# Kernel tuning notes

Measured on AMD Instinct MI355X. Metric: run time of the kernel, lower is better.

Reference implementation:

```python
import jax, jax.numpy as jnp
import numpy as np

D_MODEL = 768
NUM_HEADS = 12
HEAD_DIM = D_MODEL // NUM_HEADS
SEQ = 4096
BATCH = 1


def setup_inputs() -> dict:
    key = jax.random.key(0)
    ks = jax.random.split(key, 6)
    scale = 1.0 / np.sqrt(D_MODEL)
    x = jax.random.normal(ks[0], (BATCH, SEQ, D_MODEL), dtype=jnp.float32)
    mask = jnp.tril(jnp.ones((SEQ, SEQ), dtype=bool))[None, None]  # [1,1,S,S] causal
    Wq = jax.random.normal(ks[1], (D_MODEL, D_MODEL), dtype=jnp.float32) * scale
    Wk = jax.random.normal(ks[2], (D_MODEL, D_MODEL), dtype=jnp.float32) * scale
    Wv = jax.random.normal(ks[3], (D_MODEL, D_MODEL), dtype=jnp.float32) * scale
    Wo = jax.random.normal(ks[4], (D_MODEL, D_MODEL), dtype=jnp.float32) * scale
    bo = jax.random.normal(ks[5], (D_MODEL,), dtype=jnp.float32) * 0.01
    return {"x": x, "mask": mask, "Wq": Wq, "Wk": Wk, "Wv": Wv, "Wo": Wo, "bo": bo}


def _rope_tables(seq_len, head_dim, dtype):
    # inv_freq over even dims; emb = cat(freqs, freqs) but only the first half
    # participates in the well-defined rotation (x1/x2 have head_dim//2 channels)
    inv_freq = 1.0 / (10000.0 ** (jnp.arange(0, head_dim, 2, dtype=dtype) / head_dim))
    t = jnp.arange(seq_len, dtype=dtype)
    freqs = t[:, None] * inv_freq[None, :]  # [S, head_dim//2]
    return jnp.cos(freqs), jnp.sin(freqs)


def _apply_rotary(xh, cos, sin):
    # xh: [B,H,S,hd]; cos/sin: [S, hd//2]
    x1 = xh[..., ::2]
    x2 = xh[..., 1::2]
    # faithful to source: concatenated (not interleaved) rotated halves
    return jnp.concatenate([x1 * cos - x2 * sin, x1 * sin + x2 * cos], axis=-1)


def reference(x, mask, Wq, Wk, Wv, Wo, bo):
    B, S, D = x.shape
    H, hd = NUM_HEADS, HEAD_DIM
    def split_heads(y):
        return y.reshape(B, S, H, hd).transpose(0, 2, 1, 3)  # [B,H,S,hd]
    q = split_heads(x @ Wq.T)
    k = split_heads(x @ Wk.T)
    v = split_heads(x @ Wv.T)
    cos, sin = _rope_tables(S, hd, x.dtype)
    q = _apply_rotary(q, cos, sin)
    k = _apply_rotary(k, cos, sin)
    scores = jnp.einsum('bhqd,bhkd->bhqk', q, k) / jnp.sqrt(jnp.asarray(hd, x.dtype))
    scores = jnp.where(mask, scores, jnp.asarray(-1e9, x.dtype))
    attn = jax.nn.softmax(scores, axis=-1)  # dropout is identity in eval
    out = jnp.einsum('bhqk,bhkd->bhqd', attn, v)
    out = out.transpose(0, 2, 1, 3).reshape(B, S, D)
    return out @ Wo.T + bo
```

## Files before the change

kernel.cpp:

```cpp
#include <hip/hip_runtime.h>
#include <hip/hip_bf16.h>
#include <math.h>

#define SEQ 4096
#define DM  768
#define NH  12
#define HD  64
#define PER ((size_t)NH * SEQ * HD)
#define XN  ((size_t)SEQ * DM)
#define WN  ((size_t)DM * DM)

typedef __attribute__((ext_vector_type(8))) short bf16x8;
typedef __attribute__((ext_vector_type(4))) short s16x4;
typedef __attribute__((ext_vector_type(4))) float f32x4;

#define MFMA(a, b, c) __builtin_amdgcn_mfma_f32_16x16x32_bf16((a), (b), (c), 0, 0, 0)

#if __has_builtin(__builtin_amdgcn_exp2f)
#define EXP2(x) __builtin_amdgcn_exp2f(x)
#else
#define EXP2(x) exp2f(x)
#endif

#define SWZ(row, blk) (((row) << 6) + ((((blk) ^ ((row) & 7))) << 3))

__device__ __forceinline__ unsigned short f2b(float f) {
    unsigned int u = __float_as_uint(f);
    u += 0x7FFFu + ((u >> 16) & 1u);
    return (unsigned short)(u >> 16);
}

__global__ __launch_bounds__(256) void prep_kernel(
    const float* __restrict__ x,  const float* __restrict__ wq,
    const float* __restrict__ wk, const float* __restrict__ wv,
    const float* __restrict__ wo,
    unsigned short* __restrict__ dstbase, float2* __restrict__ rope)
{
    const float* srcs[5] = {x, wq, wk, wv, wo};
    const size_t n4s[5]  = {XN / 4, WN / 4, WN / 4, WN / 4, WN / 4};
    unsigned short* d = dstbase;
    for (int rg = 0; rg < 5; ++rg) {
        const float4* s4 = (const float4*)srcs[rg];
        s16x4* d4 = (s16x4*)d;
        for (size_t i = (size_t)blockIdx.x * 256 + threadIdx.x; i < n4s[rg];
             i += (size_t)gridDim.x * 256) {
            const float4 v = s4[i];
            s16x4 p;
            p.x = (short)f2b(v.x); p.y = (short)f2b(v.y);
            p.z = (short)f2b(v.z); p.w = (short)f2b(v.w);
            d4[i] = p;
        }
        d += n4s[rg] * 4;
    }
    for (int g = blockIdx.x * 256 + threadIdx.x; g < 131072; g += gridDim.x * 256) {
        const int row = g >> 5, fi = g & 31;
        const float invf = expf(-(float)fi * 0.28782313662425576f);
        float sn, cs;
        sincosf((float)row * invf, &sn, &cs);
        rope[row * 32 + fi] = make_float2(cs, sn);
    }
}

__global__ __launch_bounds__(256) void qkv_mfma(
    const float* __restrict__ x,  const unsigned short* __restrict__ xb,
    const float* __restrict__ Wq, const float* __restrict__ Wk, const float* __restrict__ Wv,
    const unsigned short* __restrict__ Wqb, const unsigned short* __restrict__ Wkb,
    const unsigned short* __restrict__ Wvb,
    const float2* __restrict__ rope,
    unsigned short* __restrict__ Qo, unsigned short* __restrict__ Ko,
    unsigned short* __restrict__ Vo, int fast)
{
    __shared__ __align__(16) unsigned short Xs[2][4096];
    __shared__ __align__(16) unsigned short Ws[2][4096];
    __shared__ unsigned short VL[64 * 66];

    const int t    = threadIdx.x;
    const int w    = t >> 6;
    const int lane = t & 63;
    const int quad = lane >> 4;
    const int l16  = lane & 15;

    const int nt_b = blockIdx.y;
    const float* W; const unsigned short* Wb; int region;
    if (nt_b < 12)      { W = Wq; Wb = Wqb; region = 0; }
    else if (nt_b < 24) { W = Wk; Wb = Wkb; region = 1; }
    else                { W = Wv; Wb = Wvb; region = 2; }
    const int h  = nt_b % 12;
    const int s0 = blockIdx.x * 64;
    const int n0 = h * 64;

    f32x4 acc[4] = {{0,0,0,0},{0,0,0,0},{0,0,0,0},{0,0,0,0}};
    const int prow = t >> 3, pblk = t & 7;

    bf16x8 xr0, xr1, wr0, wr1;
    if (fast) {
        xr0 = *(const bf16x8*)&xb[(size_t)(s0 + prow) * DM + pblk * 8];
        xr1 = *(const bf16x8*)&xb[(size_t)(s0 + prow + 32) * DM + pblk * 8];
        wr0 = *(const bf16x8*)&Wb[(size_t)(n0 + prow) * DM + pblk * 8];
        wr1 = *(const bf16x8*)&Wb[(size_t)(n0 + prow + 32) * DM + pblk * 8];
        *(bf16x8*)&Xs[0][SWZ(prow, pblk)]      = xr0;
        *(bf16x8*)&Xs[0][SWZ(prow + 32, pblk)] = xr1;
        *(bf16x8*)&Ws[0][SWZ(prow, pblk)]      = wr0;
        *(bf16x8*)&Ws[0][SWZ(prow + 32, pblk)] = wr1;
    } else {
        for (int e = t; e < 1024; e += 256) {
            const int row = e >> 4, c4 = e & 15;
            const int off = SWZ(row, c4 >> 1) + (c4 & 1) * 4;
            const float4 xv = *(const float4*)&x[(size_t)(s0 + row) * DM + c4 * 4];
            s16x4 px; px.x = (short)f2b(xv.x); px.y = (short)f2b(xv.y);
            px.z = (short)f2b(xv.z); px.w = (short)f2b(xv.w);
            *(s16x4*)&Xs[0][off] = px;
            const float4 wv = *(const float4*)&W[(size_t)(n0 + row) * DM + c4 * 4];
            s16x4 pw; pw.x = (short)f2b(wv.x); pw.y = (short)f2b(wv.y);
            pw.z = (short)f2b(wv.z); pw.w = (short)f2b(wv.w);
            *(s16x4*)&Ws[0][off] = pw;
        }
    }
    __syncthreads();

    for (int kt = 0; kt < 12; ++kt) {
        const unsigned short* Xb  = Xs[kt & 1];
        const unsigned short* Wbt = Ws[kt & 1];
        if (fast && kt < 11) {
            const int k0 = (kt + 1) * 64;
            xr0 = *(const bf16x8*)&xb[(size_t)(s0 + prow) * DM + k0 + pblk * 8];
            xr1 = *(const bf16x8*)&xb[(size_t)(s0 + prow + 32) * DM + k0 + pblk * 8];
            wr0 = *(const bf16x8*)&Wb[(size_t)(n0 + prow) * DM + k0 + pblk * 8];
            wr1 = *(const bf16x8*)&Wb[(size_t)(n0 + prow + 32) * DM + k0 + pblk * 8];
        }
        const bf16x8 a0 = *(const bf16x8*)&Xb[SWZ(16 * w + l16, quad)];
        const bf16x8 a1 = *(const bf16x8*)&Xb[SWZ(16 * w + l16, 4 + quad)];
        #pragma unroll
        for (int nt = 0; nt < 4; ++nt) {
            const bf16x8 b0 = *(const bf16x8*)&Wbt[SWZ(16 * nt + l16, quad)];
            const bf16x8 b1 = *(const bf16x8*)&Wbt[SWZ(16 * nt + l16, 4 + quad)];
            acc[nt] = MFMA(a0, b0, acc[nt]);
            acc[nt] = MFMA(a1, b1, acc[nt]);
        }
        if (kt < 11) {
            const int nb = (kt + 1) & 1;
            if (fast) {
                *(bf16x8*)&Xs[nb][SWZ(prow, pblk)]      = xr0;
                *(bf16x8*)&Xs[nb][SWZ(prow + 32, pblk)] = xr1;
                *(bf16x8*)&Ws[nb][SWZ(prow, pblk)]      = wr0;
                *(bf16x8*)&Ws[nb][SWZ(prow + 32, pblk)] = wr1;
            } else {
                const int k0 = (kt + 1) * 64;
                for (int e = t; e < 1024; e += 256) {
                    const int row = e >> 4, c4 = e & 15;
                    const int off = SWZ(row, c4 >> 1) + (c4 & 1) * 4;
                    const float4 xv = *(const float4*)&x[(size_t)(s0 + row) * DM + k0 + c4 * 4];
                    s16x4 px; px.x = (short)f2b(xv.x); px.y = (short)f2b(xv.y);
                    px.z = (short)f2b(xv.z); px.w = (short)f2b(xv.w);
                    *(s16x4*)&Xs[nb][off] = px;
                    const float4 wv = *(const float4*)&W[(size_t)(n0 + row) * DM + k0 + c4 * 4];
                    s16x4 pw; pw.x = (short)f2b(wv.x); pw.y = (short)f2b(wv.y);
                    pw.z = (short)f2b(wv.z); pw.w = (short)f2b(wv.w);
                    *(s16x4*)&Ws[nb][off] = pw;
                }
            }
        }
        __syncthreads();
    }

    const size_t headoff = (size_t)h * SEQ * HD;
    if (region <= 1) {
        unsigned short* dst = (region == 0) ? Qo : Ko;
        const float qsc = (region == 0) ? 0.18033688011112042f : 1.0f;
        #pragma unroll
        for (int nt = 0; nt < 4; ++nt)
            #pragma unroll
            for (int r = 0; r < 4; ++r) {
                const int srow = s0 + 16 * w + quad * 4 + r;
                const int d  = nt * 16 + l16;
                const int fi = d >> 1;
                const float own = acc[nt][r] * qsc;
                const float oth = __shfl_xor(own, 1);
                float cs, sn;
                if (fast) {
                    const float2 t2 = rope[srow * 32 + fi];
                    cs = t2.x; sn = t2.y;
                } else {
                    const float invf = expf(-(float)fi * 0.28782313662425576f);
                    sincosf((float)srow * invf, &sn, &cs);
                }
                const float val = (d & 1) ? (oth * sn + own * cs)
                                          : (own * cs - oth * sn);
                dst[headoff + (size_t)srow * HD + ((d & 1) ? 32 : 0) + fi] = f2b(val);
            }
    } else {
        #pragma unroll
        for (int nt = 0; nt < 4; ++nt)
            #pragma unroll
            for (int r = 0; r < 4; ++r)
                VL[(nt * 16 + l16) * 66 + 16 * w + quad * 4 + r] = f2b(acc[nt][r]);
        __syncthreads();
        for (int e = t; e < 2048; e += 256) {
            const int d = e >> 5, sp = e & 31;
            const unsigned int v = (unsigned int)VL[d * 66 + 2 * sp] |
                                   ((unsigned int)VL[d * 66 + 2 * sp + 1] << 16);
            *(unsigned int*)&Vo[headoff + (size_t)d * SEQ + s0 + 2 * sp] = v;
        }
    }
}

__global__ __launch_bounds__(256, 2) void attn_mfma(
    const unsigned short* __restrict__ Q,
    const unsigned short* __restrict__ K,
    const unsigned short* __restrict__ V,
    unsigned short* __restrict__ O)
{
    __shared__ __align__(16) unsigned char SM[53248];
    unsigned short* Kst = (unsigned short*)SM;
    unsigned short* Vt  = (unsigned short*)(SM + 16384);
    unsigned short* Ps  = (unsigned short*)(SM + 32768);
    float* ACC  = (float*)SM;
    float* ACC2 = (float*)(SM + 32768);
    float* Lx   = (float*)(SM + 51200);

    const int h    = blockIdx.y;
    const int q0   = (63 - blockIdx.x) * 64;
    const int t    = threadIdx.x;
    const int w    = t >> 6;
    const int lane = t & 63;
    const int quad = lane >> 4;
    const int l16  = lane & 15;
    const size_t headoff = (size_t)h * SEQ * HD;

    for (int e = t; e < 512; e += 256) {
        const int row = e >> 3, bp = e & 7, blk = bp ^ (row & 7);
        *(bf16x8*)&Kst[row * 64 + bp * 8] =
            *(const bf16x8*)&Q[headoff + (size_t)(q0 + row) * HD + blk * 8];
    }
    __syncthreads();
    bf16x8 aQ[4][2];
    #pragma unroll
    for (int qt = 0; qt < 4; ++qt)
        #pragma unroll
        for (int hh = 0; hh < 2; ++hh)
            aQ[qt][hh] = *(const bf16x8*)&Kst[SWZ(16 * qt + l16, 4 * hh + quad)];
    __syncthreads();

    bf16x8 kreg[4], vreg[4];
    #pragma unroll
    for (int i = 0; i < 4; ++i) {
        const int e = t + i * 256, row = e >> 3, bp = e & 7, blk = bp ^ (row & 7);
        kreg[i] = *(const bf16x8*)&K[headoff + (size_t)row * HD + blk * 8];
    }
    #pragma unroll
    for (int i = 0; i < 4; ++i) {
        const int e = t + i * 256, row = e >> 4, bp = e & 15, blk = bp ^ (row & 15);
        vreg[i] = *(const bf16x8*)&V[headoff + (size_t)row * SEQ + blk * 8];
    }
    #pragma unroll
    for (int i = 0; i < 4; ++i) {
        const int e = t + i * 256, row = e >> 3, bp = e & 7;
        *(bf16x8*)&Kst[row * 64 + bp * 8] = kreg[i];
    }
    #pragma unroll
    for (int i = 0; i < 4; ++i) {
        const int e = t + i * 256, row = e >> 4, bp = e & 15;
        *(bf16x8*)&Vt[row * 128 + bp * 8] = vreg[i];
    }
    __syncthreads();

    bf16x8 ones;
    #pragma unroll
    for (int i = 0; i < 8; ++i) ones[i] = (short)0x3F80;

    f32x4 oT[4][4];
    #pragma unroll
    for (int dt = 0; dt < 4; ++dt)
        #pragma unroll
        for (int qt = 0; qt < 4; ++qt) oT[dt][qt] = (f32x4){0,0,0,0};
    f32x4 lT[4] = {{0,0,0,0},{0,0,0,0},{0,0,0,0},{0,0,0,0}};

    unsigned short* usp = Ps + w * 2560;
    const int cmax = (q0 + 63) >> 7;

    for (int c = 0; c <= cmax; ++c) {
        const int k0 = c * 128;

        f32x4 sC[4][2];
        #pragma unroll
        for (int qt = 0; qt < 4; ++qt)
            #pragma unroll
            for (int kt = 0; kt < 2; ++kt) sC[qt][kt] = (f32x4){0,0,0,0};
        #pragma unroll
        for (int kt = 0; kt < 2; ++kt) {
            const int krow = 32 * w + 16 * kt + l16;
            #pragma unroll
            for (int hh = 0; hh < 2; ++hh) {
                const bf16x8 bK = *(const bf16x8*)&Kst[SWZ(krow, 4 * hh + quad)];
                #pragma unroll
                for (int qt = 0; qt < 4; ++qt)
                    sC[qt][kt] = MFMA(aQ[qt][hh], bK, sC[qt][kt]);
            }
        }

        if (c < cmax) {
            const int kn = k0 + 128;
            #pragma unroll
            for (int i = 0; i < 4; ++i) {
                const int e = t + i * 256, row = e >> 3, bp = e & 7, blk = bp ^ (row & 7);
                kreg[i] = *(const bf16x8*)&K[headoff + (size_t)(kn + row) * HD + blk * 8];
            }
            #pragma unroll
            for (int i = 0; i < 4; ++i) {
                const int e = t + i * 256, row = e >> 4, bp = e & 15, blk = bp ^ (row & 15);
                vreg[i] = *(const bf16x8*)&V[headoff + (size_t)row * SEQ + kn + blk * 8];
            }
        }

        if (c == cmax) {
            #pragma unroll
            for (int kt = 0; kt < 2; ++kt) {
                const int key = k0 + 32 * w + 16 * kt + l16;
                #pragma unroll
                for (int qt = 0; qt < 4; ++qt)
                    #pragma unroll
                    for (int r = 0; r < 4; ++r)
                        if (key > q0 + 16 * qt + 4 * quad + r) sC[qt][kt][r] = -1e30f;
            }
        }

        #pragma unroll
        for (int qt = 0; qt < 4; ++qt)
            #pragma unroll
            for (int kt = 0; kt < 2; ++kt)
                #pragma unroll
                for (int r = 0; r < 4; ++r)
                    usp[(16 * qt + 4 * quad + r) * 40 + 16 * kt + l16] =
                        f2b(EXP2(sC[qt][kt][r]));
        asm volatile("s_waitcnt lgkmcnt(0)" ::: "memory");

        bf16x8 aV[4];
        #pragma unroll
        for (int dt = 0; dt < 4; ++dt) {
            const int row = 16 * dt + l16;
            aV[dt] = *(const bf16x8*)&Vt[row * 128 + (((4 * w + quad) ^ (row & 15)) << 3)];
        }
        #pragma unroll
        for (int qt = 0; qt < 4; ++qt) {
            const bf16x8 bP = *(const bf16x8*)&usp[(16 * qt + l16) * 40 + quad * 8];
            lT[qt] = MFMA(ones, bP, lT[qt]);
            #pragma unroll
            for (int dt = 0; dt < 4; ++dt)
                oT[dt][qt] = MFMA(aV[dt], bP, oT[dt][qt]);
        }

        __syncthreads();
        if (c < cmax) {
            #pragma unroll
            for (int i = 0; i < 4; ++i) {
                const int e = t + i * 256, row = e >> 3, bp = e & 7;
                *(bf16x8*)&Kst[row * 64 + bp * 8] = kreg[i];
            }
            #pragma unroll
            for (int i = 0; i < 4; ++i) {
                const int e = t + i * 256, row = e >> 4, bp = e & 15;
                *(bf16x8*)&Vt[row * 128 + bp * 8] = vreg[i];
            }
        }
        __syncthreads();
    }

    if (w != 0 && quad == 0) {
        #pragma unroll
        for (int qt = 0; qt < 4; ++qt)
            Lx[w * 64 + 16 * qt + l16] = lT[qt][0];
    }
    if (w == 1) {
        #pragma unroll
        for (int dt = 0; dt < 4; ++dt)
            #pragma unroll
            for (int qt = 0; qt < 4; ++qt)
                *(f32x4*)&ACC[(16 * qt + l16) * 72 + 16 * dt + 4 * quad] = oT[dt][qt];
    }
    __syncthreads();
    if (w == 0) {
        #pragma unroll
        for (int dt = 0; dt < 4; ++dt)
            #pragma unroll
            for (int qt = 0; qt < 4; ++qt)
                oT[dt][qt] += *(const f32x4*)&ACC[(16 * qt + l16) * 72 + 16 * dt + 4 * quad];
    }
    if (w == 2) {
        #pragma unroll
        for (int dt = 0; dt < 4; ++dt)
            #pragma unroll
            for (int qt = 0; qt < 4; ++qt)
                *(f32x4*)&ACC2[(16 * qt + l16) * 72 + 16 * dt + 4 * quad] = oT[dt][qt];
    }
    __syncthreads();
    if (w == 0) {
        #pragma unroll
        for (int dt = 0; dt < 4; ++dt)
            #pragma unroll
            for (int qt = 0; qt < 4; ++qt)
                oT[dt][qt] += *(const f32x4*)&ACC2[(16 * qt + l16) * 72 + 16 * dt + 4 * quad];
    }
    if (w == 3) {
        #pragma unroll
        for (int dt = 0; dt < 4; ++dt)
            #pragma unroll
            for (int qt = 0; qt < 4; ++qt)
                *(f32x4*)&ACC[(16 * qt + l16) * 72 + 16 * dt + 4 * quad] = oT[dt][qt];
    }
    __syncthreads();
    if (w == 0) {
        float inv[4];
        #pragma unroll
        for (int qt = 0; qt < 4; ++qt) {
            #pragma unroll
            for (int dt = 0; dt < 4; ++dt)
                oT[dt][qt] += *(const f32x4*)&ACC[(16 * qt + l16) * 72 + 16 * dt + 4 * quad];
            const float ls = lT[qt][0] + Lx[64 + 16 * qt + l16] +
                             Lx[128 + 16 * qt + l16] + Lx[192 + 16 * qt + l16];
            inv[qt] = 1.0f / ls;
        }
        #pragma unroll
        for (int qt = 0; qt < 4; ++qt) {
            const size_t rowoff = (size_t)(q0 + 16 * qt + l16) * DM + h * HD;
            #pragma unroll
            for (int dt = 0; dt < 4; ++dt) {
                ushort4 u;
                u.x = f2b(oT[dt][qt][0] * inv[qt]);
                u.y = f2b(oT[dt][qt][1] * inv[qt]);
                u.z = f2b(oT[dt][qt][2] * inv[qt]);
                u.w = f2b(oT[dt][qt][3] * inv[qt]);
                *(ushort4*)&O[rowoff + 16 * dt + 4 * quad] = u;
            }
        }
    }
}

__global__ __launch_bounds__(256) void proj_mfma(
    const unsigned short* __restrict__ A,
    const float* __restrict__ Wo, const unsigned short* __restrict__ Wob,
    const float* __restrict__ bo,
    float* __restrict__ out, int fast)
{
    __shared__ __align__(16) unsigned short Xs[2][4096];
    __shared__ __align__(16) unsigned short Ws[2][4096];

    const int t    = threadIdx.x;
    const int w    = t >> 6;
    const int lane = t & 63;
    const int quad = lane >> 4;
    const int l16  = lane & 15;
    const int s0 = blockIdx.x * 64;
    const int n0 = blockIdx.y * 64;
    const int prow = t >> 3, pblk = t & 7;

    f32x4 acc[4] = {{0,0,0,0},{0,0,0,0},{0,0,0,0},{0,0,0,0}};

    bf16x8 ar0, ar1, wr0, wr1;
    ar0 = *(const bf16x8*)&A[(size_t)(s0 + prow) * DM + pblk * 8];
    ar1 = *(const bf16x8*)&A[(size_t)(s0 + prow + 32) * DM + pblk * 8];
    *(bf16x8*)&Xs[0][SWZ(prow, pblk)]      = ar0;
    *(bf16x8*)&Xs[0][SWZ(prow + 32, pblk)] = ar1;
    if (fast) {
        wr0 = *(const bf16x8*)&Wob[(size_t)(n0 + prow) * DM + pblk * 8];
        wr1 = *(const bf16x8*)&Wob[(size_t)(n0 + prow + 32) * DM + pblk * 8];
        *(bf16x8*)&Ws[0][SWZ(prow, pblk)]      = wr0;
        *(bf16x8*)&Ws[0][SWZ(prow + 32, pblk)] = wr1;
    } else {
        for (int e = t; e < 1024; e += 256) {
            const int row = e >> 4, c4 = e & 15;
            const float4 wv = *(const float4*)&Wo[(size_t)(n0 + row) * DM + c4 * 4];
            s16x4 pw; pw.x = (short)f2b(wv.x); pw.y = (short)f2b(wv.y);
            pw.z = (short)f2b(wv.z); pw.w = (short)f2b(wv.w);
            *(s16x4*)&Ws[0][SWZ(row, c4 >> 1) + (c4 & 1) * 4] = pw;
        }
    }
    __syncthreads();

    for (int kt = 0; kt < 12; ++kt) {
        const unsigned short* Xb  = Xs[kt & 1];
        const unsigned short* Wbt = Ws[kt & 1];
        if (kt < 11) {
            const int k0 = (kt + 1) * 64;
            ar0 = *(const bf16x8*)&A[(size_t)(s0 + prow) * DM + k0 + pblk * 8];
            ar1 = *(const bf16x8*)&A[(size_t)(s0 + prow + 32) * DM + k0 + pblk * 8];
            if (fast) {
                wr0 = *(const bf16x8*)&Wob[(size_t)(n0 + prow) * DM + k0 + pblk * 8];
                wr1 = *(const bf16x8*)&Wob[(size_t)(n0 + prow + 32) * DM + k0 + pblk * 8];
            }
        }
        const bf16x8 a0 = *(const bf16x8*)&Xb[SWZ(16 * w + l16, quad)];
        const bf16x8 a1 = *(const bf16x8*)&Xb[SWZ(16 * w + l16, 4 + quad)];
        #pragma unroll
        for (int nt = 0; nt < 4; ++nt) {
            const bf16x8 b0 = *(const bf16x8*)&Wbt[SWZ(16 * nt + l16, quad)];
            const bf16x8 b1 = *(const bf16x8*)&Wbt[SWZ(16 * nt + l16, 4 + quad)];
            acc[nt] = MFMA(a0, b0, acc[nt]);
            acc[nt] = MFMA(a1, b1, acc[nt]);
        }
        if (kt < 11) {
            const int nb = (kt + 1) & 1;
            *(bf16x8*)&Xs[nb][SWZ(prow, pblk)]      = ar0;
            *(bf16x8*)&Xs[nb][SWZ(prow + 32, pblk)] = ar1;
            if (fast) {
                *(bf16x8*)&Ws[nb][SWZ(prow, pblk)]      = wr0;
                *(bf16x8*)&Ws[nb][SWZ(prow + 32, pblk)] = wr1;
            } else {
                const int k0 = (kt + 1) * 64;
                for (int e = t; e < 1024; e += 256) {
                    const int row = e >> 4, c4 = e & 15;
                    const float4 wv = *(const float4*)&Wo[(size_t)(n0 + row) * DM + k0 + c4 * 4];
                    s16x4 pw; pw.x = (short)f2b(wv.x); pw.y = (short)f2b(wv.y);
                    pw.z = (short)f2b(wv.z); pw.w = (short)f2b(wv.w);
                    *(s16x4*)&Ws[nb][SWZ(row, c4 >> 1) + (c4 & 1) * 4] = pw;
                }
            }
        }
        __syncthreads();
    }

    #pragma unroll
    for (int nt = 0; nt < 4; ++nt)
        #pragma unroll
        for (int r = 0; r < 4; ++r) {
            const int srow = s0 + 16 * w + quad * 4 + r;
            const int n    = n0 + nt * 16 + l16;
            out[(size_t)srow * DM + n] = acc[nt][r] + bo[n];
        }
}

extern "C" void kernel_launch(void* const* d_in, const int* in_sizes, int n_in,
                              void* d_out, int out_size, void* d_ws, size_t ws_size,
                              hipStream_t stream) {
    const float* x  = (const float*)d_in[0];
    const float* Wq = (const float*)d_in[2];
    const float* Wk = (const float*)d_in[3];
    const float* Wv = (const float*)d_in[4];
    const float* Wo = (const float*)d_in[5];
    const float* bo = (const float*)d_in[6];
    float* out = (float*)d_out;

    unsigned short* U  = (unsigned short*)d_ws;
    unsigned short* Qw = U;
    unsigned short* Kw = U + PER;
    unsigned short* Vw = U + 2 * PER;
    unsigned short* Ow = U + 3 * PER;
    unsigned short* xb  = U + 4 * PER;
    unsigned short* Wqb = xb + XN;
    unsigned short* Wkb = Wqb + WN;
    unsigned short* Wvb = Wkb + WN;
    unsigned short* Wob = Wvb + WN;
    float2* rope = (float2*)(Wob + WN);
    const size_t need = (char*)(rope + 4096 * 32) - (char*)d_ws;
    const int fast = (ws_size >= need) ? 1 : 0;

    if (fast)
        prep_kernel<<<1024, 256, 0, stream>>>(x, Wq, Wk, Wv, Wo, xb, rope);
    qkv_mfma<<<dim3(SEQ / 64, 36), 256, 0, stream>>>(
        x, xb, Wq, Wk, Wv, Wqb, Wkb, Wvb, rope, Qw, Kw, Vw, fast);
    attn_mfma<<<dim3(SEQ / 64, NH), 256, 0, stream>>>(Qw, Kw, Vw, Ow);
    proj_mfma<<<dim3(SEQ / 64, DM / 64), 256, 0, stream>>>(Ow, Wo, Wob, bo, out, fast);
}
```

Baseline: 248.8 us.

## Split long causal attention rows across two key ranges with a reduce kernel

Query blocks in the upper half of the sequence have their key range split into two slices, [0,2048) and [2048,end), each handled by its own workgroup. The grid grows from 64 to 96 blocks per head. Partial unnormalized outputs and row sums go to a workspace buffer, and a new reduce kernel combines and normalizes them. This evens out the triangular work imbalance and raises parallelism, at the cost of an extra launch plus fp32 partial writes and reads. The sum-only combine is exact only because the kernel never subtracts a running max.

```diff
diff --git a/kernel.cpp b/kernel.cpp
--- a/kernel.cpp
+++ b/kernel.cpp
@@ -208,7 +208,8 @@
     const unsigned short* __restrict__ Q,
     const unsigned short* __restrict__ K,
     const unsigned short* __restrict__ V,
-    unsigned short* __restrict__ O)
+    unsigned short* __restrict__ O,
+    float* __restrict__ Part)
 {
     __shared__ __align__(16) unsigned char SM[53248];
     unsigned short* Kst = (unsigned short*)SM;
@@ -218,8 +219,28 @@
     float* ACC2 = (float*)(SM + 32768);
     float* Lx   = (float*)(SM + 51200);
 
-    const int h    = blockIdx.y;
-    const int q0   = (63 - blockIdx.x) * 64;
+    const int h  = blockIdx.y;
+    const int xx = blockIdx.x;
+    int i, kstart, nch, domask, partial, pslice;
+    if (gridDim.x == 96) {
+        if (xx < 64) {
+            i = 63 - xx; kstart = 0;
+            const int full = ((i * 64 + 63) >> 7) + 1;
+            nch = full < 16 ? full : 16;
+            domask  = (i <= 31);
+            partial = (i >= 32); pslice = 0;
+        } else {
+            i = 127 - xx; kstart = 2048;
+            nch = ((i * 64 + 63 - 2048) >> 7) + 1;
+            domask = 1; partial = 1; pslice = 1;
+        }
+    } else {
+        i = 63 - xx; kstart = 0;
+        nch = ((i * 64 + 63) >> 7) + 1;
+        domask = 1; partial = 0; pslice = 0;
+    }
+    const int q0 = i * 64;
+
     const int t    = threadIdx.x;
     const int w    = t >> 6;
     const int lane = t & 63;
@@ -243,30 +264,30 @@
 
     bf16x8 kreg[4], vreg[4];
     #pragma unroll
-    for (int i = 0; i < 4; ++i) {
-        const int e = t + i * 256, row = e >> 3, bp = e & 7, blk = bp ^ (row & 7);
-        kreg[i] = *(const bf16x8*)&K[headoff + (size_t)row * HD + blk * 8];
-    }
-    #pragma unroll
-    for (int i = 0; i < 4; ++i) {
-        const int e = t + i * 256, row = e >> 4, bp = e & 15, blk = bp ^ (row & 15);
-        vreg[i] = *(const bf16x8*)&V[headoff + (size_t)row * SEQ + blk * 8];
-    }
-    #pragma unroll
-    for (int i = 0; i < 4; ++i) {
-        const int e = t + i * 256, row = e >> 3, bp = e & 7;
-        *(bf16x8*)&Kst[row * 64 + bp * 8] = kreg[i];
-    }
-    #pragma unroll
-    for (int i = 0; i < 4; ++i) {
-        const int e = t + i * 256, row = e >> 4, bp = e & 15;
-        *(bf16x8*)&Vt[row * 128 + bp * 8] = vreg[i];
+    for (int ii = 0; ii < 4; ++ii) {
+        const int e = t + ii * 256, row = e >> 3, bp = e & 7, blk = bp ^ (row & 7);
+        kreg[ii] = *(const bf16x8*)&K[headoff + (size_t)(kstart + row) * HD + blk * 8];
+    }
+    #pragma unroll
+    for (int ii = 0; ii < 4; ++ii) {
+        const int e = t + ii * 256, row = e >> 4, bp = e & 15, blk = bp ^ (row & 15);
+        vreg[ii] = *(const bf16x8*)&V[headoff + (size_t)row * SEQ + kstart + blk * 8];
+    }
+    #pragma unroll
+    for (int ii = 0; ii < 4; ++ii) {
+        const int e = t + ii * 256, row = e >> 3, bp = e & 7;
+        *(bf16x8*)&Kst[row * 64 + bp * 8] = kreg[ii];
+    }
+    #pragma unroll
+    for (int ii = 0; ii < 4; ++ii) {
+        const int e = t + ii * 256, row = e >> 4, bp = e & 15;
+        *(bf16x8*)&Vt[row * 128 + bp * 8] = vreg[ii];
     }
     __syncthreads();
 
     bf16x8 ones;
     #pragma unroll
-    for (int i = 0; i < 8; ++i) ones[i] = (short)0x3F80;
+    for (int ii = 0; ii < 8; ++ii) ones[ii] = (short)0x3F80;
 
     f32x4 oT[4][4];
     #pragma unroll
@@ -276,10 +297,9 @@
     f32x4 lT[4] = {{0,0,0,0},{0,0,0,0},{0,0,0,0},{0,0,0,0}};
 
     unsigned short* usp = Ps + w * 2560;
-    const int cmax = (q0 + 63) >> 7;
-
-    for (int c = 0; c <= cmax; ++c) {
-        const int k0 = c * 128;
+
+    for (int c = 0; c < nch; ++c) {
+        const int k0 = kstart + c * 128;
 
         f32x4 sC[4][2];
         #pragma unroll
@@ -298,21 +318,21 @@
             }
         }
 
-        if (c < cmax) {
+        if (c < nch - 1) {
             const int kn = k0 + 128;
             #pragma unroll
-            for (int i = 0; i < 4; ++i) {
-                const int e = t + i * 256, row = e >> 3, bp = e & 7, blk = bp ^ (row & 7);
-                kreg[i] = *(const bf16x8*)&K[headoff + (size_t)(kn + row) * HD + blk * 8];
-            }
-            #pragma unroll
-            for (int i = 0; i < 4; ++i) {
-                const int e = t + i * 256, row = e >> 4, bp = e & 15, blk = bp ^ (row & 15);
-                vreg[i] = *(const bf16x8*)&V[headoff + (size_t)row * SEQ + kn + blk * 8];
-            }
-        }
-
-        if (c == cmax) {
+            for (int ii = 0; ii < 4; ++ii) {
+                const int e = t + ii * 256, row = e >> 3, bp = e & 7, blk = bp ^ (row & 7);
+                kreg[ii] = *(const bf16x8*)&K[headoff + (size_t)(kn + row) * HD + blk * 8];
+            }
+            #pragma unroll
+            for (int ii = 0; ii < 4; ++ii) {
+                const int e = t + ii * 256, row = e >> 4, bp = e & 15, blk = bp ^ (row & 15);
+                vreg[ii] = *(const bf16x8*)&V[headoff + (size_t)row * SEQ + kn + blk * 8];
+            }
+        }
+
+        if (domask && c == nch - 1) {
             #pragma unroll
             for (int kt = 0; kt < 2; ++kt) {
                 const int key = k0 + 32 * w + 16 * kt + l16;
@@ -350,16 +370,16 @@
         }
 
         __syncthreads();
-        if (c < cmax) {
-            #pragma unroll
-            for (int i = 0; i < 4; ++i) {
-                const int e = t + i * 256, row = e >> 3, bp = e & 7;
-                *(bf16x8*)&Kst[row * 64 + bp * 8] = kreg[i];
-            }
-            #pragma unroll
-            for (int i = 0; i < 4; ++i) {
-                const int e = t + i * 256, row = e >> 4, bp = e & 15;
-                *(bf16x8*)&Vt[row * 128 + bp * 8] = vreg[i];
+        if (c < nch - 1) {
+            #pragma unroll
+            for (int ii = 0; ii < 4; ++ii) {
+                const int e = t + ii * 256, row = e >> 3, bp = e & 7;
+                *(bf16x8*)&Kst[row * 64 + bp * 8] = kreg[ii];
+            }
+            #pragma unroll
+            for (int ii = 0; ii < 4; ++ii) {
+                const int e = t + ii * 256, row = e >> 4, bp = e & 15;
+                *(bf16x8*)&Vt[row * 128 + bp * 8] = vreg[ii];
             }
         }
         __syncthreads();
@@ -409,29 +429,62 @@
     }
     __syncthreads();
     if (w == 0) {
-        float inv[4];
+        float ls[4];
         #pragma unroll
         for (int qt = 0; qt < 4; ++qt) {
             #pragma unroll
             for (int dt = 0; dt < 4; ++dt)
                 oT[dt][qt] += *(const f32x4*)&ACC[(16 * qt + l16) * 72 + 16 * dt + 4 * quad];
-            const float ls = lT[qt][0] + Lx[64 + 16 * qt + l16] +
-                             Lx[128 + 16 * qt + l16] + Lx[192 + 16 * qt + l16];
-            inv[qt] = 1.0f / ls;
-        }
-        #pragma unroll
-        for (int qt = 0; qt < 4; ++qt) {
-            const size_t rowoff = (size_t)(q0 + 16 * qt + l16) * DM + h * HD;
-            #pragma unroll
-            for (int dt = 0; dt < 4; ++dt) {
-                ushort4 u;
-                u.x = f2b(oT[dt][qt][0] * inv[qt]);
-                u.y = f2b(oT[dt][qt][1] * inv[qt]);
-                u.z = f2b(oT[dt][qt][2] * inv[qt]);
-                u.w = f2b(oT[dt][qt][3] * inv[qt]);
-                *(ushort4*)&O[rowoff + 16 * dt + 4 * quad] = u;
-            }
-        }
+            ls[qt] = lT[qt][0] + Lx[64 + 16 * qt + l16] +
+                     Lx[128 + 16 * qt + l16] + Lx[192 + 16 * qt + l16];
+        }
+        if (!partial) {
+            #pragma unroll
+            for (int qt = 0; qt < 4; ++qt) {
+                const float inv = 1.0f / ls[qt];
+                const size_t rowoff = (size_t)(q0 + 16 * qt + l16) * DM + h * HD;
+                #pragma unroll
+                for (int dt = 0; dt < 4; ++dt) {
+                    ushort4 u;
+                    u.x = f2b(oT[dt][qt][0] * inv);
+                    u.y = f2b(oT[dt][qt][1] * inv);
+                    u.z = f2b(oT[dt][qt][2] * inv);
+                    u.w = f2b(oT[dt][qt][3] * inv);
+                    *(ushort4*)&O[rowoff + 16 * dt + 4 * quad] = u;
+                }
+            }
+        } else {
+            float* P = Part + (size_t)(((i - 32) * 12 + h) * 2 + pslice) * 4160;
+            #pragma unroll
+            for (int dt = 0; dt < 4; ++dt)
+                #pragma unroll
+                for (int qt = 0; qt < 4; ++qt)
+                    *(f32x4*)&P[(16 * qt + l16) * 64 + 16 * dt + 4 * quad] = oT[dt][qt];
+            if (quad == 0) {
+                #pragma unroll
+                for (int qt = 0; qt < 4; ++qt)
+                    P[4096 + 16 * qt + l16] = ls[qt];
+            }
+        }
+    }
+}
+
+__global__ __launch_bounds__(256) void reduce_attn(
+    const float* __restrict__ Part, unsigned short* __restrict__ O)
+{
+    const int b  = blockIdx.x;
+    const int i  = 32 + b / 12, h = b % 12;
+    const int q0 = i * 64;
+    const float* P0 = Part + (size_t)(b * 2 + 0) * 4160;
+    const float* P1 = Part + (size_t)(b * 2 + 1) * 4160;
+    __shared__ float linv[64];
+    const int t = threadIdx.x;
+    if (t < 64) linv[t] = 1.0f / (P0[4096 + t] + P1[4096 + t]);
+    __syncthreads();
+    for (int idx = t; idx < 4096; idx += 256) {
+        const int q = idx >> 6, d = idx & 63;
+        const float v = (P0[q * 64 + d] + P1[q * 64 + d]) * linv[q];
+        O[(size_t)(q0 + q) * DM + h * HD + d] = f2b(v);
     }
 }
 
@@ -550,13 +603,21 @@
     unsigned short* Wvb = Wkb + WN;
     unsigned short* Wob = Wvb + WN;
     float2* rope = (float2*)(Wob + WN);
-    const size_t need = (char*)(rope + 4096 * 32) - (char*)d_ws;
-    const int fast = (ws_size >= need) ? 1 : 0;
+    float*  part = (float*)(rope + 4096 * 32);
+    const size_t need  = (char*)part - (char*)d_ws;
+    const size_t need2 = need + (size_t)384 * 2 * 4160 * 4;
+    const int fast  = (ws_size >= need)  ? 1 : 0;
+    const int split = (ws_size >= need2) ? 1 : 0;
 
     if (fast)
         prep_kernel<<<1024, 256, 0, stream>>>(x, Wq, Wk, Wv, Wo, xb, rope);
     qkv_mfma<<<dim3(SEQ / 64, 36), 256, 0, stream>>>(
         x, xb, Wq, Wk, Wv, Wqb, Wkb, Wvb, rope, Qw, Kw, Vw, fast);
-    attn_mfma<<<dim3(SEQ / 64, NH), 256, 0, stream>>>(Qw, Kw, Vw, Ow);
+    if (split) {
+        attn_mfma<<<dim3(96, NH), 256, 0, stream>>>(Qw, Kw, Vw, Ow, part);
+        reduce_attn<<<dim3(384), 256, 0, stream>>>(part, Ow);
+    } else {
+        attn_mfma<<<dim3(64, NH), 256, 0, stream>>>(Qw, Kw, Vw, Ow, part);
+    }
     proj_mfma<<<dim3(SEQ / 64, DM / 64), 256, 0, stream>>>(Ow, Wo, Wob, bo, out, fast);
 }
```

Result: faster. 243.3 us (-2.2%).
